# Performance work log

Hardware: AMD Instinct MI355X
Metric: run time of the kernel (lower is better)

Reference implementation:

```python
import jax, jax.numpy as jnp
import numpy as np
import math

N_NODES = 50000
N_EDGES = 800000
NFEAT = 512
NHID = 128
NCLASS = 128
NLAYERS = 16
LAMDA = 0.5
ALPHA = 0.1


def setup_inputs() -> dict:
    key = jax.random.key(0)
    k1, k2, k3, k4, k5, k6, k7, k8 = jax.random.split(key, 8)
    x = jax.random.normal(k1, (N_NODES, NFEAT), dtype=jnp.float32)
    # edges with no self loops: col = (row + offset) % N, offset in [1, N)
    row = jax.random.randint(k2, (N_EDGES,), 0, N_NODES, dtype=jnp.int32)
    off = jax.random.randint(k3, (N_EDGES,), 1, N_NODES, dtype=jnp.int32)
    col = (row + off) % N_NODES
    edge_idx = jnp.stack([row, col], axis=0)
    # conv weights: uniform(-stdv, stdv), stdv = 1/sqrt(out_features)
    stdv = 1.0 / math.sqrt(NHID)
    conv_w = jax.random.uniform(k4, (NLAYERS, NHID, NHID), jnp.float32, -stdv, stdv)
    # fc layers (stored as [in, out]; equivalent to torch Linear y = x @ W.T + b)
    fc0_w = jax.random.normal(k5, (NFEAT, NHID), jnp.float32) * (1.0 / math.sqrt(NFEAT))
    fc0_b = jax.random.normal(k6, (NHID,), jnp.float32) * 0.01
    fc1_w = jax.random.normal(k7, (NHID, NCLASS), jnp.float32) * (1.0 / math.sqrt(NHID))
    fc1_b = jax.random.normal(k8, (NCLASS,), jnp.float32) * 0.01
    return {"x": x, "edge_idx": edge_idx, "conv_w": conv_w,
            "fc0_w": fc0_w, "fc0_b": fc0_b, "fc1_w": fc1_w, "fc1_b": fc1_b}


def reference(x, edge_idx, conv_w, fc0_w, fc0_b, fc1_w, fc1_b):
    # eval mode: dropout is identity
    n = x.shape[0]
    loop = jnp.arange(n, dtype=edge_idx.dtype)
    # add_remaining_self_loops: inputs have no self loops -> append unit loops
    row = jnp.concatenate([edge_idx[0], loop])
    col = jnp.concatenate([edge_idx[1], loop])
    w = jnp.ones(row.shape[0], dtype=x.dtype)
    # symmetric normalization: D^-1/2 A D^-1/2
    deg = jax.ops.segment_sum(w, row, num_segments=n)
    dinv = jnp.where(deg > 0, jax.lax.rsqrt(deg), 0.0).astype(x.dtype)
    w = dinv[row] * w * dinv[col]

    h0 = jax.nn.relu(x @ fc0_w + fc0_b)  # [N, NHID]
    thetas = jnp.log(LAMDA / jnp.arange(1, NLAYERS + 1, dtype=x.dtype) + 1.0)

    def layer(h, wt):
        Wl, theta = wt
        # SpMM: hi[r] = sum_{(r,c) in E} w_rc * h[c]
        hi = jax.ops.segment_sum(w[:, None] * h[col], row, num_segments=n)
        support = (1.0 - ALPHA) * hi + ALPHA * h0
        out = theta * (support @ Wl) + (1.0 - theta) * support
        return jax.nn.relu(out), None

    h, _ = jax.lax.scan(layer, h0, (conv_w, thetas))
    return h @ fc1_w + fc1_b  # [N, NCLASS]
```

## Files before the change

### kernel.cpp

```cpp
#include <hip/hip_runtime.h>
#include <hip/hip_bf16.h>
#include <math.h>

#define N_NODES_C 50000
#define N_EDGES_C 800000
#define NFEAT_C 512
#define NH_C 128
#define NLAYERS_C 16
#define LDB 136

typedef __attribute__((ext_vector_type(8))) short short8;
typedef __attribute__((ext_vector_type(4))) float f32x4;

__device__ __forceinline__ float b2f(unsigned short h) {
    union { unsigned int u; float f; } v; v.u = ((unsigned int)h) << 16; return v.f;
}
__device__ __forceinline__ unsigned short f2b(float f) {
    union { float f; unsigned int u; } v; v.f = f;
    unsigned int r = (v.u + 0x7fffu + ((v.u >> 16) & 1u)) >> 16;
    return (unsigned short)r;
}


__global__ __launch_bounds__(256) void k_count(const int* __restrict__ row,
                                               int* __restrict__ cnt) {
    int e = blockIdx.x * 256 + threadIdx.x;
    atomicAdd(&cnt[row[e]], 1);
}

__global__ __launch_bounds__(256) void k_scan1(const int* __restrict__ cnt,
                                               int* __restrict__ locex,
                                               int* __restrict__ partials, int n) {
    __shared__ int sm[256];
    int t = threadIdx.x;
    int i = blockIdx.x * 256 + t;
    int v = (i < n) ? cnt[i] : 0;
    sm[t] = v;
    __syncthreads();
    for (int o = 1; o < 256; o <<= 1) {
        int x = (t >= o) ? sm[t - o] : 0;
        __syncthreads();
        sm[t] += x;
        __syncthreads();
    }
    if (i < n) locex[i] = sm[t] - v;
    if (t == 255) partials[blockIdx.x] = sm[255];
}

__global__ __launch_bounds__(256) void k_scan2(int* __restrict__ partials, int np) {
    __shared__ int sm[256];
    int t = threadIdx.x;
    int v = (t < np) ? partials[t] : 0;
    sm[t] = v;
    __syncthreads();
    for (int o = 1; o < 256; o <<= 1) {
        int x = (t >= o) ? sm[t - o] : 0;
        __syncthreads();
        sm[t] += x;
        __syncthreads();
    }
    if (t < np) partials[t] = sm[t] - v;
}

__global__ __launch_bounds__(256) void k_scan3(const int* __restrict__ cnt,
                                               const int* __restrict__ locex,
                                               const int* __restrict__ partials,
                                               int* __restrict__ rowptr,
                                               int* __restrict__ cursor,
                                               float* __restrict__ dinv,
                                               int n, int ne) {
    int i = blockIdx.x * 256 + threadIdx.x;
    if (i < n) {
        int rp = locex[i] + partials[i >> 8];
        rowptr[i] = rp;
        cursor[i] = rp;
        dinv[i] = 1.0f / sqrtf((float)(cnt[i] + 1));
    }
    if (i == 0) rowptr[n] = ne;
}

__global__ __launch_bounds__(256) void k_fill(const int* __restrict__ row,
                                              const int* __restrict__ col,
                                              int* __restrict__ cursor,
                                              int* __restrict__ colsorted) {
    int e = blockIdx.x * 256 + threadIdx.x;
    int p = atomicAdd(&cursor[row[e]], 1);
    colsorted[p] = col[e];
}


__global__ __launch_bounds__(256) void k_convt128(const float* __restrict__ src,
                                                  unsigned short* __restrict__ dst,
                                                  int total) {
    int i = blockIdx.x * 256 + threadIdx.x;
    if (i >= total) return;
    int l = i >> 14, w = i & 16383;
    int n = w >> 7, k = w & 127;
    dst[i] = f2b(src[(l << 14) + (k << 7) + n]);
}

__global__ __launch_bounds__(256) void k_convt_fc0(const float* __restrict__ src,
                                                   unsigned short* __restrict__ dst) {
    int i = blockIdx.x * 256 + threadIdx.x;
    int n = i >> 9, k = i & 511;
    dst[i] = f2b(src[(k << 7) + n]);
}


__device__ __forceinline__ void acc8(float* a, uint4 u) {
    a[0] += b2f((unsigned short)(u.x & 0xffffu));
    a[1] += b2f((unsigned short)(u.x >> 16));
    a[2] += b2f((unsigned short)(u.y & 0xffffu));
    a[3] += b2f((unsigned short)(u.y >> 16));
    a[4] += b2f((unsigned short)(u.z & 0xffffu));
    a[5] += b2f((unsigned short)(u.z >> 16));
    a[6] += b2f((unsigned short)(u.w & 0xffffu));
    a[7] += b2f((unsigned short)(u.w >> 16));
}

__global__ __launch_bounds__(256) void k_spmm(const unsigned short* __restrict__ hs,
                                              const unsigned short* __restrict__ h0,
                                              const float* __restrict__ dinv,
                                              const int* __restrict__ rowptr,
                                              const int* __restrict__ cols,
                                              unsigned short* __restrict__ sout) {
    const int w = threadIdx.x >> 6, ln = threadIdx.x & 63;
    const int r = blockIdx.x * 4 + w;
    const int g = ln >> 4, gi = ln & 15;
    const uint4* hs4 = (const uint4*)hs;
    const uint4* h04 = (const uint4*)h0;

    float a[8];
#pragma unroll
    for (int j = 0; j < 8; j++) a[j] = 0.f;

    int e = rowptr[r];
    const int end = rowptr[r + 1];

    if (g == 0) {
        uint4 u = hs4[(size_t)r * 16 + gi];
        acc8(a, u);
    }
    for (; e + 15 < end; e += 16) {
        int cA = cols[e + g];
        int cB = cols[e + 4 + g];
        int cC = cols[e + 8 + g];
        int cD = cols[e + 12 + g];
        uint4 uA = hs4[(size_t)cA * 16 + gi];
        uint4 uB = hs4[(size_t)cB * 16 + gi];
        uint4 uC = hs4[(size_t)cC * 16 + gi];
        uint4 uD = hs4[(size_t)cD * 16 + gi];
        acc8(a, uA);
        acc8(a, uB);
        acc8(a, uC);
        acc8(a, uD);
    }
    for (; e + 3 < end; e += 4) {
        int c = cols[e + g];
        uint4 u = hs4[(size_t)c * 16 + gi];
        acc8(a, u);
    }
    int rem = end - e;
    if (g < rem) {
        int c = cols[e + g];
        uint4 u = hs4[(size_t)c * 16 + gi];
        acc8(a, u);
    }

#pragma unroll
    for (int j = 0; j < 8; j++) {
        a[j] += __shfl_xor(a[j], 16);
        a[j] += __shfl_xor(a[j], 32);
    }

    float dr = 0.9f * dinv[r];
    uint4 hv = h04[(size_t)r * 16 + gi];
    uint4 o;
    o.x = (unsigned int)f2b(dr * a[0] + 0.1f * b2f((unsigned short)(hv.x & 0xffffu))) |
          ((unsigned int)f2b(dr * a[1] + 0.1f * b2f((unsigned short)(hv.x >> 16))) << 16);
    o.y = (unsigned int)f2b(dr * a[2] + 0.1f * b2f((unsigned short)(hv.y & 0xffffu))) |
          ((unsigned int)f2b(dr * a[3] + 0.1f * b2f((unsigned short)(hv.y >> 16))) << 16);
    o.z = (unsigned int)f2b(dr * a[4] + 0.1f * b2f((unsigned short)(hv.z & 0xffffu))) |
          ((unsigned int)f2b(dr * a[5] + 0.1f * b2f((unsigned short)(hv.z >> 16))) << 16);
    o.w = (unsigned int)f2b(dr * a[6] + 0.1f * b2f((unsigned short)(hv.w & 0xffffu))) |
          ((unsigned int)f2b(dr * a[7] + 0.1f * b2f((unsigned short)(hv.w >> 16))) << 16);
    if (g == 0) ((uint4*)sout)[(size_t)r * 16 + gi] = o;
}


__global__ __launch_bounds__(256) void k_gemm_blend(
    const unsigned short* __restrict__ S, const float* __restrict__ dinv,
    const unsigned short* __restrict__ WT, unsigned short* __restrict__ hdst,
    float theta, int use_dinv) {
    __shared__ __align__(16) unsigned short s_lds[64 * LDB];
    __shared__ __align__(16) unsigned short bt[128 * LDB];
    const int tid = threadIdx.x;
    const int w = tid >> 6, ln = tid & 63;
    const int quad = ln >> 4, l16 = ln & 15;
    const int block_base = blockIdx.x * 64;

    for (int chunk = tid; chunk < 128 * 16; chunk += 256) {
        int n = chunk >> 4, k8 = (chunk & 15) << 3;
        *(short8*)&bt[n * LDB + k8] = *(const short8*)&WT[(n << 7) + k8];
    }
    for (int chunk = tid; chunk < 64 * 16; chunk += 256) {
        int n = chunk >> 4, k8 = (chunk & 15) << 3;
        int row = block_base + n;
        short8 v = {};
        if (row < N_NODES_C) v = *(const short8*)&S[(size_t)row * NH_C + k8];
        *(short8*)&s_lds[n * LDB + k8] = v;
    }
    __syncthreads();

    f32x4 acc[8];
#pragma unroll
    for (int j = 0; j < 8; j++) acc[j] = (f32x4){0.f, 0.f, 0.f, 0.f};
#pragma unroll
    for (int ki = 0; ki < 128; ki += 32) {
        short8 af = *(const short8*)&s_lds[((w << 4) + l16) * LDB + ki + quad * 8];
#pragma unroll
        for (int nt = 0; nt < 8; nt++) {
            short8 bf = *(const short8*)&bt[(nt * 16 + l16) * LDB + ki + quad * 8];
            acc[nt] = __builtin_amdgcn_mfma_f32_16x16x32_bf16(af, bf, acc[nt], 0, 0, 0);
        }
    }

#pragma unroll
    for (int reg = 0; reg < 4; reg++) {
        int lr = (w << 4) + (quad << 2) + reg;
        int r = block_base + lr;
        float drv = dinv[(r < N_NODES_C) ? r : (N_NODES_C - 1)];
#pragma unroll
        for (int nt = 0; nt < 8; nt++) {
            int n = nt * 16 + l16;
            float s = b2f(s_lds[lr * LDB + n]);
            float v = theta * acc[nt][reg] + (1.f - theta) * s;
            v = fmaxf(v, 0.f);
            if (use_dinv) v *= drv;
            s_lds[lr * LDB + n] = f2b(v);
        }
    }
    __syncthreads();
    for (int chunk = tid; chunk < 64 * 16; chunk += 256) {
        int lr = chunk >> 4, c8 = (chunk & 15) << 3;
        int row = block_base + lr;
        if (row < N_NODES_C)
            *(short8*)&hdst[(size_t)row * NH_C + c8] = *(const short8*)&s_lds[lr * LDB + c8];
    }
}


template <int AFP32, int MT>
__global__ __launch_bounds__(256) void k_gemm(
    const void* __restrict__ Av, const unsigned short* __restrict__ WT,
    int M, int K,
    const float* __restrict__ bias, const float* __restrict__ dinv,
    unsigned short* __restrict__ out0, unsigned short* __restrict__ out1,
    float* __restrict__ outf, int mode) {
    __shared__ __align__(16) unsigned short bt[128 * LDB];
    const int tid = threadIdx.x;
    const int w = tid >> 6, ln = tid & 63;
    const int quad = ln >> 4, l16 = ln & 15;
    const int ROWS = 64 * MT;
    const int block_base = blockIdx.x * ROWS;
    const int m_base = block_base + w * (16 * MT);

    f32x4 acc[MT][8];
#pragma unroll
    for (int i = 0; i < MT; i++)
#pragma unroll
        for (int j = 0; j < 8; j++) acc[i][j] = (f32x4){0.f, 0.f, 0.f, 0.f};

    for (int kc = 0; kc < K; kc += 128) {
        for (int chunk = tid; chunk < 128 * 16; chunk += 256) {
            int n = chunk >> 4, k8 = (chunk & 15) << 3;
            *(short8*)&bt[n * LDB + k8] = *(const short8*)&WT[(size_t)n * K + kc + k8];
        }
        __syncthreads();
#pragma unroll
        for (int ki = 0; ki < 128; ki += 32) {
            short8 bf[8];
#pragma unroll
            for (int nt = 0; nt < 8; nt++)
                bf[nt] = *(const short8*)&bt[(nt * 16 + l16) * LDB + ki + quad * 8];
#pragma unroll
            for (int mt = 0; mt < MT; mt++) {
                int row = m_base + mt * 16 + l16;
                if (row >= M) row = M - 1;
                short8 af;
                if (AFP32) {
                    const float* A = (const float*)Av;
                    const float* p = &A[(size_t)row * K + kc + ki + quad * 8];
                    float4 f0 = *(const float4*)p;
                    float4 f1 = *(const float4*)(p + 4);
                    af[0] = (short)f2b(f0.x); af[1] = (short)f2b(f0.y);
                    af[2] = (short)f2b(f0.z); af[3] = (short)f2b(f0.w);
                    af[4] = (short)f2b(f1.x); af[5] = (short)f2b(f1.y);
                    af[6] = (short)f2b(f1.z); af[7] = (short)f2b(f1.w);
                } else {
                    const unsigned short* A = (const unsigned short*)Av;
                    af = *(const short8*)&A[(size_t)row * K + kc + ki + quad * 8];
                }
#pragma unroll
                for (int nt = 0; nt < 8; nt++)
                    acc[mt][nt] = __builtin_amdgcn_mfma_f32_16x16x32_bf16(
                        af, bf[nt], acc[mt][nt], 0, 0, 0);
            }
        }
        __syncthreads();
    }

    if (mode == 2) {
#pragma unroll
        for (int mt = 0; mt < MT; mt++)
#pragma unroll
            for (int reg = 0; reg < 4; reg++) {
                int r = m_base + mt * 16 + quad * 4 + reg;
                if (r >= M) continue;
#pragma unroll
                for (int nt = 0; nt < 8; nt++) {
                    int n = nt * 16 + l16;
                    outf[(size_t)r * NH_C + n] = acc[mt][nt][reg] + bias[n];
                }
            }
        return;
    }

#pragma unroll
    for (int mt = 0; mt < MT; mt++)
#pragma unroll
        for (int reg = 0; reg < 4; reg++) {
            int lr = w * (16 * MT) + mt * 16 + quad * 4 + reg;
#pragma unroll
            for (int nt = 0; nt < 8; nt++) {
                int n = nt * 16 + l16;
                float v = acc[mt][nt][reg] + bias[n];
                bt[lr * LDB + n] = f2b(fmaxf(v, 0.f));
            }
        }
    __syncthreads();
    for (int chunk = tid; chunk < ROWS * 16; chunk += 256) {
        int lr = chunk >> 4, c8 = (chunk & 15) << 3;
        int row = block_base + lr;
        if (row >= M) continue;
        short8 v = *(const short8*)&bt[lr * LDB + c8];
        *(short8*)&out1[(size_t)row * NH_C + c8] = v;
        float dr = dinv[row];
        short8 o;
#pragma unroll
        for (int j = 0; j < 8; j++)
            o[j] = (short)f2b(b2f((unsigned short)v[j]) * dr);
        *(short8*)&out0[(size_t)row * NH_C + c8] = o;
    }
}


extern "C" void kernel_launch(void* const* d_in, const int* in_sizes, int n_in,
                              void* d_out, int out_size, void* d_ws, size_t ws_size,
                              hipStream_t stream) {
    const float* x = (const float*)d_in[0];
    const int* edge = (const int*)d_in[1];
    const float* convw = (const float*)d_in[2];
    const float* fc0w = (const float*)d_in[3];
    const float* fc0b = (const float*)d_in[4];
    const float* fc1w = (const float*)d_in[5];
    const float* fc1b = (const float*)d_in[6];
    const int* erow = edge;
    const int* ecol = edge + N_EDGES_C;

    char* ws = (char*)d_ws;
    size_t off = 0;
    auto alloc = [&](size_t bytes) -> void* {
        off = (off + 255) & ~(size_t)255;
        void* p = ws + off;
        off += bytes;
        return p;
    };
    int* cnt = (int*)alloc(N_NODES_C * 4);
    int* cursor = (int*)alloc(N_NODES_C * 4);
    int* locex = (int*)alloc(N_NODES_C * 4);
    int* partials = (int*)alloc(1024);
    int* rowptr = (int*)alloc((N_NODES_C + 1) * 4);
    float* dinv = (float*)alloc(N_NODES_C * 4);
    int* colsorted = (int*)alloc(N_EDGES_C * 4);
    unsigned short* wconvT = (unsigned short*)alloc((size_t)NLAYERS_C * NH_C * NH_C * 2);
    unsigned short* wfc0T = (unsigned short*)alloc((size_t)NFEAT_C * NH_C * 2);
    unsigned short* wfc1T = (unsigned short*)alloc((size_t)NH_C * NH_C * 2);
    unsigned short* h0 = (unsigned short*)alloc((size_t)N_NODES_C * NH_C * 2);
    unsigned short* hsA = (unsigned short*)alloc((size_t)N_NODES_C * NH_C * 2);
    unsigned short* hsB = (unsigned short*)alloc((size_t)N_NODES_C * NH_C * 2);
    unsigned short* sbuf = (unsigned short*)alloc((size_t)N_NODES_C * NH_C * 2);
    (void)ws_size; (void)n_in; (void)in_sizes; (void)out_size;

    k_convt128<<<NLAYERS_C * NH_C * NH_C / 256, 256, 0, stream>>>(
        convw, wconvT, NLAYERS_C * NH_C * NH_C);
    k_convt_fc0<<<NFEAT_C * NH_C / 256, 256, 0, stream>>>(fc0w, wfc0T);
    k_convt128<<<NH_C * NH_C / 256, 256, 0, stream>>>(fc1w, wfc1T, NH_C * NH_C);

    hipMemsetAsync(cnt, 0, N_NODES_C * 4, stream);
    k_count<<<N_EDGES_C / 256, 256, 0, stream>>>(erow, cnt);
    const int NB = (N_NODES_C + 255) / 256;
    k_scan1<<<NB, 256, 0, stream>>>(cnt, locex, partials, N_NODES_C);
    k_scan2<<<1, 256, 0, stream>>>(partials, NB);
    k_scan3<<<NB, 256, 0, stream>>>(cnt, locex, partials, rowptr, cursor, dinv,
                                    N_NODES_C, N_EDGES_C);
    k_fill<<<N_EDGES_C / 256, 256, 0, stream>>>(erow, ecol, cursor, colsorted);

    const int GB1 = (N_NODES_C + 63) / 64;
    k_gemm<1, 1><<<GB1, 256, 0, stream>>>(x, wfc0T, N_NODES_C, NFEAT_C, fc0b, dinv,
                                          hsA, h0, nullptr, 0);
    unsigned short* cur = hsA;
    unsigned short* nxt = hsB;
    for (int l = 0; l < NLAYERS_C; l++) {
        k_spmm<<<N_NODES_C / 4, 256, 0, stream>>>(cur, h0, dinv, rowptr, colsorted,
                                                  sbuf);
        float theta = logf(0.5f / (float)(l + 1) + 1.0f);
        k_gemm_blend<<<GB1, 256, 0, stream>>>(sbuf, dinv,
                                              wconvT + (size_t)l * NH_C * NH_C, nxt,
                                              theta, (l < NLAYERS_C - 1) ? 1 : 0);
        unsigned short* t = cur; cur = nxt; nxt = t;
    }
    k_gemm<0, 1><<<GB1, 256, 0, stream>>>(cur, wfc1T, N_NODES_C, NH_C, fc1b, dinv,
                                          nullptr, nullptr, (float*)d_out, 2);
}
```

Baseline: 1.006 ms.

## Split SpMM feature dimension across grid and read GEMM weights from global

The SpMM kernel now splits the 128-wide feature row into four column slices along a second grid dimension. Each wave handles one slice of a row with 16 edge groups of 4 lanes, which raises edge-level parallelism per wave and adds two more shuffle-reduction steps. The blend GEMM no longer stages the weight matrix in LDS and reads B fragments straight from global/L2. This shrinks LDS use per block, which may raise occupancy, at the cost of uncoalesced repeated global loads. The column index reads are now repeated across four blocks per row.

```diff
diff --git a/kernel.cpp b/kernel.cpp
--- a/kernel.cpp
+++ b/kernel.cpp
@@ -126,7 +126,8 @@
                                               unsigned short* __restrict__ sout) {
     const int w = threadIdx.x >> 6, ln = threadIdx.x & 63;
     const int r = blockIdx.x * 4 + w;
-    const int g = ln >> 4, gi = ln & 15;
+    const int g = ln >> 2, gi = ln & 3;
+    const int sbase = blockIdx.y * 4;
     const uint4* hs4 = (const uint4*)hs;
     const uint4* h04 = (const uint4*)h0;
 
@@ -137,44 +138,35 @@
     int e = rowptr[r];
     const int end = rowptr[r + 1];
 
-    if (g == 0) {
-        uint4 u = hs4[(size_t)r * 16 + gi];
-        acc8(a, u);
+    if (g == 0) acc8(a, hs4[(size_t)r * 16 + sbase + gi]);
+
+    for (; e + 31 < end; e += 32) {
+        int c0 = cols[e + g];
+        int c1 = cols[e + 16 + g];
+        uint4 u0 = hs4[(size_t)c0 * 16 + sbase + gi];
+        uint4 u1 = hs4[(size_t)c1 * 16 + sbase + gi];
+        acc8(a, u0);
+        acc8(a, u1);
     }
     for (; e + 15 < end; e += 16) {
-        int cA = cols[e + g];
-        int cB = cols[e + 4 + g];
-        int cC = cols[e + 8 + g];
-        int cD = cols[e + 12 + g];
-        uint4 uA = hs4[(size_t)cA * 16 + gi];
-        uint4 uB = hs4[(size_t)cB * 16 + gi];
-        uint4 uC = hs4[(size_t)cC * 16 + gi];
-        uint4 uD = hs4[(size_t)cD * 16 + gi];
-        acc8(a, uA);
-        acc8(a, uB);
-        acc8(a, uC);
-        acc8(a, uD);
-    }
-    for (; e + 3 < end; e += 4) {
         int c = cols[e + g];
-        uint4 u = hs4[(size_t)c * 16 + gi];
-        acc8(a, u);
-    }
-    int rem = end - e;
-    if (g < rem) {
+        acc8(a, hs4[(size_t)c * 16 + sbase + gi]);
+    }
+    if (e + g < end) {
         int c = cols[e + g];
-        uint4 u = hs4[(size_t)c * 16 + gi];
-        acc8(a, u);
+        acc8(a, hs4[(size_t)c * 16 + sbase + gi]);
     }
 
 #pragma unroll
     for (int j = 0; j < 8; j++) {
+        a[j] += __shfl_xor(a[j], 4);
+        a[j] += __shfl_xor(a[j], 8);
         a[j] += __shfl_xor(a[j], 16);
         a[j] += __shfl_xor(a[j], 32);
     }
 
     float dr = 0.9f * dinv[r];
-    uint4 hv = h04[(size_t)r * 16 + gi];
+    uint4 hv = h04[(size_t)r * 16 + sbase + gi];
     uint4 o;
     o.x = (unsigned int)f2b(dr * a[0] + 0.1f * b2f((unsigned short)(hv.x & 0xffffu))) |
           ((unsigned int)f2b(dr * a[1] + 0.1f * b2f((unsigned short)(hv.x >> 16))) << 16);
@@ -184,7 +176,7 @@
           ((unsigned int)f2b(dr * a[5] + 0.1f * b2f((unsigned short)(hv.z >> 16))) << 16);
     o.w = (unsigned int)f2b(dr * a[6] + 0.1f * b2f((unsigned short)(hv.w & 0xffffu))) |
           ((unsigned int)f2b(dr * a[7] + 0.1f * b2f((unsigned short)(hv.w >> 16))) << 16);
-    if (g == 0) ((uint4*)sout)[(size_t)r * 16 + gi] = o;
+    if (g == 0) ((uint4*)sout)[(size_t)r * 16 + sbase + gi] = o;
 }
 
 
@@ -193,16 +185,11 @@
     const unsigned short* __restrict__ WT, unsigned short* __restrict__ hdst,
     float theta, int use_dinv) {
     __shared__ __align__(16) unsigned short s_lds[64 * LDB];
-    __shared__ __align__(16) unsigned short bt[128 * LDB];
     const int tid = threadIdx.x;
     const int w = tid >> 6, ln = tid & 63;
     const int quad = ln >> 4, l16 = ln & 15;
     const int block_base = blockIdx.x * 64;
 
-    for (int chunk = tid; chunk < 128 * 16; chunk += 256) {
-        int n = chunk >> 4, k8 = (chunk & 15) << 3;
-        *(short8*)&bt[n * LDB + k8] = *(const short8*)&WT[(n << 7) + k8];
-    }
     for (int chunk = tid; chunk < 64 * 16; chunk += 256) {
         int n = chunk >> 4, k8 = (chunk & 15) << 3;
         int row = block_base + n;
@@ -220,7 +207,7 @@
         short8 af = *(const short8*)&s_lds[((w << 4) + l16) * LDB + ki + quad * 8];
 #pragma unroll
         for (int nt = 0; nt < 8; nt++) {
-            short8 bf = *(const short8*)&bt[(nt * 16 + l16) * LDB + ki + quad * 8];
+            short8 bf = *(const short8*)&WT[((nt * 16 + l16) << 7) + ki + quad * 8];
             acc[nt] = __builtin_amdgcn_mfma_f32_16x16x32_bf16(af, bf, acc[nt], 0, 0, 0);
         }
     }
@@ -412,8 +399,8 @@
     unsigned short* cur = hsA;
     unsigned short* nxt = hsB;
     for (int l = 0; l < NLAYERS_C; l++) {
-        k_spmm<<<N_NODES_C / 4, 256, 0, stream>>>(cur, h0, dinv, rowptr, colsorted,
-                                                  sbuf);
+        k_spmm<<<dim3(N_NODES_C / 4, 4), 256, 0, stream>>>(cur, h0, dinv, rowptr,
+                                                           colsorted, sbuf);
         float theta = logf(0.5f / (float)(l + 1) + 1.0f);
         k_gemm_blend<<<GB1, 256, 0, stream>>>(sbuf, dinv,
                                               wconvT + (size_t)l * NH_C * NH_C, nxt,
```

After: 1.875 ms. 86.3% more time.
